# Kernel optimization log

Hardware: AMD Instinct MI355X
Metric: run time of the kernel (lower is better)

Reference implementation:

```python
import math
import jax, jax.numpy as jnp
import numpy as np

B, S, D, L = 8, 4096, 1024, 16

def setup_inputs() -> dict:
    key = jax.random.key(0)
    k1, k2, k3 = jax.random.split(key, 3)
    memory = jax.random.normal(k1, (B, S, D), dtype=jnp.float32)
    summarizer = jax.random.normal(k2, (L, D), dtype=jnp.float32) * 0.02
    w_proj = jax.random.normal(k3, (1, L), dtype=jnp.float32) * (1.0 / math.sqrt(L))
    return {"memory": memory, "summarizer": summarizer, "w_proj": w_proj}

def reference(memory, summarizer, w_proj):
    # scores: [B, L, S] = summarizer @ memory^T / sqrt(D)
    d = summarizer.shape[-1]
    scores = jnp.einsum('ld,bsd->bls', summarizer, memory) / jnp.sqrt(jnp.asarray(d, memory.dtype))
    p_attn = jax.nn.softmax(scores, axis=-1)            # softmax over sequence S
    ctx = jnp.einsum('bls,bsd->bld', p_attn, memory)    # [B, L, D]
    # nn.Linear(L, 1, bias=False) applied to ctx.transpose(-1,-2): [B, D, L] @ W^T -> [B, D, 1]
    out = jnp.einsum('bld,l->bd', ctx, w_proj[0])       # [B, D]
    return out[:, None, :]                              # [B, 1, D] after final transpose
```

## Files before the change

### kernel.cpp

```cpp
#include <hip/hip_runtime.h>

#define SS 4096
#define DD 1024
#define LL 16
#define ROWF 1028

typedef __attribute__((ext_vector_type(8))) short short8;
typedef __attribute__((ext_vector_type(4))) float fl4;

static __device__ __forceinline__ short f2bf(float f) {
    unsigned u = __float_as_uint(f);
    u += 0x7FFFu + ((u >> 16) & 1u);
    return (short)(u >> 16);
}

static __device__ __forceinline__ short8 pack8(fl4 a, fl4 b) {
    short8 r;
    r[0] = f2bf(a[0]); r[1] = f2bf(a[1]); r[2] = f2bf(a[2]); r[3] = f2bf(a[3]);
    r[4] = f2bf(b[0]); r[5] = f2bf(b[1]); r[6] = f2bf(b[2]); r[7] = f2bf(b[3]);
    return r;
}

static __device__ __forceinline__ void dma16(const float* g, float* l) {
    __builtin_amdgcn_global_load_lds(
        (const __attribute__((address_space(1))) void*)g,
        (__attribute__((address_space(3))) void*)l, 16, 0, 0);
}

__global__ __launch_bounds__(512) void k_main(const float* __restrict__ mem,
                                              const float* __restrict__ summ,
                                              float* __restrict__ part,
                                              float* __restrict__ Zpart) {
    __shared__ float buf[2][16 * ROWF];
    __shared__ float e_lds[16 * LL];
    __shared__ float scr[8][256];

    int blk = blockIdx.x;
    int b   = blk >> 5;
    int s_base = (blk & 31) << 7;
    int t    = threadIdx.x;
    int wv   = t >> 6;
    int lane = t & 63;
    int o  = lane & 15;
    int qd = lane >> 4;

    const float* gseg = mem + ((size_t)b * SS + s_base) * DD;

    fl4 a0[4], a1[4];
    {
        const float* arow = summ + o * DD + wv * 128 + qd * 8;
        #pragma unroll
        for (int j = 0; j < 4; ++j) {
            a0[j] = *(const fl4*)(arow + j * 32);
            a1[j] = *(const fl4*)(arow + j * 32 + 4);
        }
    }

    #pragma unroll
    for (int r = 0; r < 2; ++r) {
        int row = wv * 2 + r;
        #pragma unroll
        for (int c = 0; c < 4; ++c)
            dma16(gseg + (size_t)row * DD + c * 256 + lane * 4,
                  &buf[0][row * ROWF + c * 256]);
    }

    short8 afr[4];
    #pragma unroll
    for (int j = 0; j < 4; ++j) afr[j] = pack8(a0[j], a1[j]);

    int lg = t >> 8;
    int q  = t & 255;
    int s_sm = t & 15;
    int l_sm = (t >> 4) & 15;
    int scr_idx = ((l_sm >> 2) * 16 + s_sm) * 4 + (l_sm & 3);

    fl4 ctx[8];
    #pragma unroll
    for (int l = 0; l < 8; ++l) ctx[l] = (fl4){0.f, 0.f, 0.f, 0.f};
    float z = 0.f;
    const float scale = 0.03125f;

    for (int p = 0; p < 8; ++p) {
        asm volatile("s_waitcnt lgkmcnt(0)" ::: "memory");
        __builtin_amdgcn_s_barrier();
        __builtin_amdgcn_sched_barrier(0);

        if (p < 7) {
            float* nbuf = &buf[(p + 1) & 1][0];
            const float* gp = gseg + (size_t)(p + 1) * 16 * DD;
            #pragma unroll
            for (int r = 0; r < 2; ++r) {
                int row = wv * 2 + r;
                #pragma unroll
                for (int c = 0; c < 4; ++c)
                    dma16(gp + (size_t)row * DD + c * 256 + lane * 4,
                          &nbuf[row * ROWF + c * 256]);
            }
            asm volatile("s_waitcnt vmcnt(8)" ::: "memory");
        } else {
            asm volatile("s_waitcnt vmcnt(0)" ::: "memory");
        }
        __builtin_amdgcn_sched_barrier(0);
        __builtin_amdgcn_s_barrier();
        __builtin_amdgcn_sched_barrier(0);

        const float* bbase = &buf[p & 1][0];
        fl4 acc = {0.f, 0.f, 0.f, 0.f};
        const float* brow = bbase + o * ROWF + wv * 128 + qd * 8;
        #pragma unroll
        for (int j = 0; j < 4; ++j) {
            fl4 f0 = *(const fl4*)(brow + j * 32);
            fl4 f1 = *(const fl4*)(brow + j * 32 + 4);
            acc = __builtin_amdgcn_mfma_f32_16x16x32_bf16(afr[j], pack8(f0, f1),
                                                          acc, 0, 0, 0);
        }
        *(fl4*)&scr[wv][lane * 4] = acc;
        asm volatile("s_waitcnt lgkmcnt(0)" ::: "memory");
        __builtin_amdgcn_s_barrier();
        __builtin_amdgcn_sched_barrier(0);

        if (t < 256) {
            float sum = 0.f;
            #pragma unroll
            for (int w = 0; w < 8; ++w) sum += scr[w][scr_idx];
            float ev = __expf(sum * scale);
            e_lds[s_sm * LL + l_sm] = ev;
            z += ev;
        }
        asm volatile("s_waitcnt lgkmcnt(0)" ::: "memory");
        __builtin_amdgcn_s_barrier();
        __builtin_amdgcn_sched_barrier(0);

        const float* mrow = bbase + q * 4;
        const fl4* erow = (const fl4*)&e_lds[lg * 8];
        #pragma unroll 4
        for (int s = 0; s < 16; ++s) {
            fl4 m4 = *(const fl4*)(mrow + s * ROWF);
            fl4 e0 = erow[s * 4];
            fl4 e1 = erow[s * 4 + 1];
            #pragma unroll
            for (int j = 0; j < 4; ++j) {
                ctx[j]     += e0[j] * m4;
                ctx[4 + j] += e1[j] * m4;
            }
        }
    }

    float* pp = part + (size_t)blk * LL * DD + (size_t)(lg * 8) * DD + q * 4;
    #pragma unroll
    for (int l = 0; l < 8; ++l) *(fl4*)(pp + (size_t)l * DD) = ctx[l];

    if (t < 256) {
        float v = z;
        v += __shfl_xor(v, 1, 64);
        v += __shfl_xor(v, 2, 64);
        v += __shfl_xor(v, 4, 64);
        v += __shfl_xor(v, 8, 64);
        if (s_sm == 0) Zpart[blk * LL + l_sm] = v;
    }
}

__global__ __launch_bounds__(256) void k_out(const float* __restrict__ part,
                                             const float* __restrict__ Zpart,
                                             const float* __restrict__ w,
                                             float* __restrict__ out) {
    int blkid = blockIdx.x;
    int b  = blkid >> 5;
    int d0 = (blkid & 31) << 5;
    int t = threadIdx.x;
    __shared__ float coef[LL];
    __shared__ fl4 red[32][8];

    if (t < LL) {
        float Z = 0.f;
        #pragma unroll
        for (int s = 0; s < 32; ++s) Z += Zpart[(b * 32 + s) * LL + t];
        coef[t] = w[t] / Z;
    }
    __syncthreads();

    int dq  = t & 7;
    int seg = t >> 3;
    const float* pb = part + (size_t)(b * 32 + seg) * LL * DD + d0 + dq * 4;
    fl4 acc = {0.f, 0.f, 0.f, 0.f};
    #pragma unroll
    for (int l = 0; l < LL; ++l) {
        fl4 v = *(const fl4*)(pb + (size_t)l * DD);
        float c = coef[l];
        acc += c * v;
    }
    red[seg][dq] = acc;
    __syncthreads();

    if (t < 8) {
        fl4 s = {0.f, 0.f, 0.f, 0.f};
        #pragma unroll
        for (int g = 0; g < 32; ++g) s += red[g][t];
        *(fl4*)&out[b * DD + d0 + t * 4] = s;
    }
}

extern "C" void kernel_launch(void* const* d_in, const int* in_sizes, int n_in,
                              void* d_out, int out_size, void* d_ws, size_t ws_size,
                              hipStream_t stream) {
    const float* mem  = (const float*)d_in[0];
    const float* summ = (const float*)d_in[1];
    const float* w    = (const float*)d_in[2];
    float* out = (float*)d_out;

    char* ws = (char*)d_ws;
    float* Zpart = (float*)ws;
    float* part  = (float*)(ws + 64 * 1024);

    k_main<<<256, 512, 0, stream>>>(mem, summ, part, Zpart);
    k_out<<<256, 256, 0, stream>>>(part, Zpart, w, out);
}
```

Before: 204.4 us.

## Fuse main and output kernels via cooperative grid sync and atomic accumulation

Merges the two kernels into one cooperative launch. After a grid-wide sync on the softmax partial sums, each block scales its register-resident context by w/Z and atomically adds it into the output. This removes the write and re-read of the large per-block context buffer and the second kernel launch. In exchange it adds grid-sync latency, float atomics whose summation order is nondeterministic, and a dependency on all 256 blocks being co-resident.

```diff
diff --git a/kernel.cpp b/kernel.cpp
--- a/kernel.cpp
+++ b/kernel.cpp
@@ -1,4 +1,7 @@
 #include <hip/hip_runtime.h>
+#include <hip/hip_cooperative_groups.h>
+
+namespace cg = cooperative_groups;
 
 #define SS 4096
 #define DD 1024
@@ -27,13 +30,15 @@
         (__attribute__((address_space(3))) void*)l, 16, 0, 0);
 }
 
-__global__ __launch_bounds__(512) void k_main(const float* __restrict__ mem,
-                                              const float* __restrict__ summ,
-                                              float* __restrict__ part,
-                                              float* __restrict__ Zpart) {
+__global__ __launch_bounds__(512) void k_fused(const float* __restrict__ mem,
+                                               const float* __restrict__ summ,
+                                               const float* __restrict__ w,
+                                               float* __restrict__ out,
+                                               float* __restrict__ Zpart) {
     __shared__ float buf[2][16 * ROWF];
     __shared__ float e_lds[16 * LL];
     __shared__ float scr[8][256];
+    __shared__ float coef[LL];
 
     int blk = blockIdx.x;
     int b   = blk >> 5;
@@ -55,6 +60,8 @@
             a1[j] = *(const fl4*)(arow + j * 32 + 4);
         }
     }
+
+    if (blk < 8 && t < 256) *(fl4*)(out + blk * DD + t * 4) = (fl4){0.f, 0.f, 0.f, 0.f};
 
     #pragma unroll
     for (int r = 0; r < 2; ++r) {
@@ -123,7 +130,7 @@
         if (t < 256) {
             float sum = 0.f;
             #pragma unroll
-            for (int w = 0; w < 8; ++w) sum += scr[w][scr_idx];
+            for (int w8 = 0; w8 < 8; ++w8) sum += scr[w8][scr_idx];
             float ev = __expf(sum * scale);
             e_lds[s_sm * LL + l_sm] = ev;
             z += ev;
@@ -147,10 +154,6 @@
         }
     }
 
-    float* pp = part + (size_t)blk * LL * DD + (size_t)(lg * 8) * DD + q * 4;
-    #pragma unroll
-    for (int l = 0; l < 8; ++l) *(fl4*)(pp + (size_t)l * DD) = ctx[l];
-
     if (t < 256) {
         float v = z;
         v += __shfl_xor(v, 1, 64);
@@ -159,18 +162,8 @@
         v += __shfl_xor(v, 8, 64);
         if (s_sm == 0) Zpart[blk * LL + l_sm] = v;
     }
-}
 
-__global__ __launch_bounds__(256) void k_out(const float* __restrict__ part,
-                                             const float* __restrict__ Zpart,
-                                             const float* __restrict__ w,
-                                             float* __restrict__ out) {
-    int blkid = blockIdx.x;
-    int b  = blkid >> 5;
-    int d0 = (blkid & 31) << 5;
-    int t = threadIdx.x;
-    __shared__ float coef[LL];
-    __shared__ fl4 red[32][8];
+    cg::this_grid().sync();
 
     if (t < LL) {
         float Z = 0.f;
@@ -180,25 +173,15 @@
     }
     __syncthreads();
 
-    int dq  = t & 7;
-    int seg = t >> 3;
-    const float* pb = part + (size_t)(b * 32 + seg) * LL * DD + d0 + dq * 4;
-    fl4 acc = {0.f, 0.f, 0.f, 0.f};
+    fl4 wsum = {0.f, 0.f, 0.f, 0.f};
     #pragma unroll
-    for (int l = 0; l < LL; ++l) {
-        fl4 v = *(const fl4*)(pb + (size_t)l * DD);
-        float c = coef[l];
-        acc += c * v;
-    }
-    red[seg][dq] = acc;
-    __syncthreads();
+    for (int l = 0; l < 8; ++l) wsum += coef[lg * 8 + l] * ctx[l];
 
-    if (t < 8) {
-        fl4 s = {0.f, 0.f, 0.f, 0.f};
-        #pragma unroll
-        for (int g = 0; g < 32; ++g) s += red[g][t];
-        *(fl4*)&out[b * DD + d0 + t * 4] = s;
-    }
+    float* op = out + (size_t)b * DD + q * 4;
+    atomicAdd(op + 0, wsum[0]);
+    atomicAdd(op + 1, wsum[1]);
+    atomicAdd(op + 2, wsum[2]);
+    atomicAdd(op + 3, wsum[3]);
 }
 
 extern "C" void kernel_launch(void* const* d_in, const int* in_sizes, int n_in,
@@ -208,11 +191,9 @@
     const float* summ = (const float*)d_in[1];
     const float* w    = (const float*)d_in[2];
     float* out = (float*)d_out;
+    float* Zpart = (float*)d_ws;
 
-    char* ws = (char*)d_ws;
-    float* Zpart = (float*)ws;
-    float* part  = (float*)(ws + 64 * 1024);
-
-    k_main<<<256, 512, 0, stream>>>(mem, summ, part, Zpart);
-    k_out<<<256, 256, 0, stream>>>(part, Zpart, w, out);
+    void* args[] = {(void*)&mem, (void*)&summ, (void*)&w, (void*)&out, (void*)&Zpart};
+    hipLaunchCooperativeKernel((const void*)k_fused, dim3(256), dim3(512),
+                               args, 0, stream);
 }
```

New measurement: 251.4 us. +23.0%, slower.

## Deepen LDS pipeline to four 8-row stages with three tiles in flight

Applied to the files above, without the earlier changes.

Splits each 16-row tile into 8-row chunks and uses a 4-deep LDS ring buffer with three prefetches outstanding instead of double buffering. The context accumulation for the previous chunk is moved to the top of the next iteration so it overlaps the wait for loads, and one barrier per iteration is dropped. The MFMA now computes only 8 useful score rows of 16, which wastes half the matrix work, and halving the chunk size doubles the number of iterations and barriers.

```diff
diff --git a/kernel.cpp b/kernel.cpp
--- a/kernel.cpp
+++ b/kernel.cpp
@@ -31,8 +31,8 @@
                                               const float* __restrict__ summ,
                                               float* __restrict__ part,
                                               float* __restrict__ Zpart) {
-    __shared__ float buf[2][16 * ROWF];
-    __shared__ float e_lds[16 * LL];
+    __shared__ float buf[4][8 * ROWF];
+    __shared__ float e_lds[8 * LL];
     __shared__ float scr[8][256];
 
     int blk = blockIdx.x;
@@ -55,24 +55,23 @@
             a1[j] = *(const fl4*)(arow + j * 32 + 4);
         }
     }
-
-    #pragma unroll
-    for (int r = 0; r < 2; ++r) {
-        int row = wv * 2 + r;
+    short8 afr[4];
+    #pragma unroll
+    for (int j = 0; j < 4; ++j) afr[j] = pack8(a0[j], a1[j]);
+
+    #pragma unroll
+    for (int g0 = 0; g0 < 3; ++g0) {
+        const float* gp = gseg + (size_t)g0 * 8 * DD;
         #pragma unroll
         for (int c = 0; c < 4; ++c)
-            dma16(gseg + (size_t)row * DD + c * 256 + lane * 4,
-                  &buf[0][row * ROWF + c * 256]);
-    }
-
-    short8 afr[4];
-    #pragma unroll
-    for (int j = 0; j < 4; ++j) afr[j] = pack8(a0[j], a1[j]);
+            dma16(gp + (size_t)wv * DD + c * 256 + lane * 4,
+                  &buf[g0][wv * ROWF + c * 256]);
+    }
 
     int lg = t >> 8;
     int q  = t & 255;
-    int s_sm = t & 15;
-    int l_sm = (t >> 4) & 15;
+    int s_sm = t & 7;
+    int l_sm = (t >> 3) & 15;
     int scr_idx = ((l_sm >> 2) * 16 + s_sm) * 4 + (l_sm & 3);
 
     fl4 ctx[8];
@@ -81,33 +80,42 @@
     float z = 0.f;
     const float scale = 0.03125f;
 
-    for (int p = 0; p < 8; ++p) {
+    for (int g = 0; g < 16; ++g) {
+        if (g > 0) {
+            const float* mrow = &buf[(g - 1) & 3][0] + q * 4;
+            const fl4* erow = (const fl4*)&e_lds[lg * 8];
+            #pragma unroll
+            for (int s = 0; s < 8; ++s) {
+                fl4 m4 = *(const fl4*)(mrow + s * ROWF);
+                fl4 e0 = erow[s * 4];
+                fl4 e1 = erow[s * 4 + 1];
+                #pragma unroll
+                for (int j = 0; j < 4; ++j) {
+                    ctx[j]     += e0[j] * m4;
+                    ctx[4 + j] += e1[j] * m4;
+                }
+            }
+        }
         asm volatile("s_waitcnt lgkmcnt(0)" ::: "memory");
+        if (g <= 13)      asm volatile("s_waitcnt vmcnt(8)" ::: "memory");
+        else if (g == 14) asm volatile("s_waitcnt vmcnt(4)" ::: "memory");
+        else              asm volatile("s_waitcnt vmcnt(0)" ::: "memory");
+        __builtin_amdgcn_sched_barrier(0);
         __builtin_amdgcn_s_barrier();
         __builtin_amdgcn_sched_barrier(0);
 
-        if (p < 7) {
-            float* nbuf = &buf[(p + 1) & 1][0];
-            const float* gp = gseg + (size_t)(p + 1) * 16 * DD;
-            #pragma unroll
-            for (int r = 0; r < 2; ++r) {
-                int row = wv * 2 + r;
-                #pragma unroll
-                for (int c = 0; c < 4; ++c)
-                    dma16(gp + (size_t)row * DD + c * 256 + lane * 4,
-                          &nbuf[row * ROWF + c * 256]);
-            }
-            asm volatile("s_waitcnt vmcnt(8)" ::: "memory");
-        } else {
-            asm volatile("s_waitcnt vmcnt(0)" ::: "memory");
-        }
-        __builtin_amdgcn_sched_barrier(0);
-        __builtin_amdgcn_s_barrier();
-        __builtin_amdgcn_sched_barrier(0);
-
-        const float* bbase = &buf[p & 1][0];
+        if (g <= 12) {
+            const float* gp = gseg + (size_t)(g + 3) * 8 * DD;
+            dma16(gp + (size_t)wv * DD +   0 + lane * 4, &buf[(g + 3) & 3][wv * ROWF +   0]);
+            dma16(gp + (size_t)wv * DD + 256 + lane * 4, &buf[(g + 3) & 3][wv * ROWF + 256]);
+            dma16(gp + (size_t)wv * DD + 512 + lane * 4, &buf[(g + 3) & 3][wv * ROWF + 512]);
+            dma16(gp + (size_t)wv * DD + 768 + lane * 4, &buf[(g + 3) & 3][wv * ROWF + 768]);
+        }
+        __builtin_amdgcn_sched_barrier(0);
+
+        const float* bbase = &buf[g & 3][0];
         fl4 acc = {0.f, 0.f, 0.f, 0.f};
-        const float* brow = bbase + o * ROWF + wv * 128 + qd * 8;
+        const float* brow = bbase + (o & 7) * ROWF + wv * 128 + qd * 8;
         #pragma unroll
         for (int j = 0; j < 4; ++j) {
             fl4 f0 = *(const fl4*)(brow + j * 32);
@@ -120,10 +128,10 @@
         __builtin_amdgcn_s_barrier();
         __builtin_amdgcn_sched_barrier(0);
 
-        if (t < 256) {
+        if (t < 128) {
             float sum = 0.f;
             #pragma unroll
-            for (int w = 0; w < 8; ++w) sum += scr[w][scr_idx];
+            for (int w8 = 0; w8 < 8; ++w8) sum += scr[w8][scr_idx];
             float ev = __expf(sum * scale);
             e_lds[s_sm * LL + l_sm] = ev;
             z += ev;
@@ -131,11 +139,13 @@
         asm volatile("s_waitcnt lgkmcnt(0)" ::: "memory");
         __builtin_amdgcn_s_barrier();
         __builtin_amdgcn_sched_barrier(0);
-
-        const float* mrow = bbase + q * 4;
+    }
+
+    {
+        const float* mrow = &buf[15 & 3][0] + q * 4;
         const fl4* erow = (const fl4*)&e_lds[lg * 8];
-        #pragma unroll 4
-        for (int s = 0; s < 16; ++s) {
+        #pragma unroll
+        for (int s = 0; s < 8; ++s) {
             fl4 m4 = *(const fl4*)(mrow + s * ROWF);
             fl4 e0 = erow[s * 4];
             fl4 e1 = erow[s * 4 + 1];
@@ -151,12 +161,11 @@
     #pragma unroll
     for (int l = 0; l < 8; ++l) *(fl4*)(pp + (size_t)l * DD) = ctx[l];
 
-    if (t < 256) {
+    if (t < 128) {
         float v = z;
         v += __shfl_xor(v, 1, 64);
         v += __shfl_xor(v, 2, 64);
         v += __shfl_xor(v, 4, 64);
-        v += __shfl_xor(v, 8, 64);
         if (s_sm == 0) Zpart[blk * LL + l_sm] = v;
     }
 }
```

Result: slower. 209.9 us (+2.7%).
